# Performance work log

Measured on AMD Instinct MI355X. Metric: run time of the kernel, lower is better.

## Reference

```python
import jax, jax.numpy as jnp
import numpy as np

B, S, H, F, K = 32, 512, 256, 256, 3
NBINS, MAX_MEL = 256, 2048


def _conv1d(x, w, b):
    # x: [B,S,Cin], w: [K,Cin,Cout] -> [B,S,Cout], padding 1 (SAME, k=3)
    return jax.lax.conv_general_dilated(x, w, (1,), 'SAME',
        dimension_numbers=('NWC', 'WIO', 'NWC')) + b


def _ln(x, g, b):
    m = jnp.mean(x, -1, keepdims=True)
    v = jnp.var(x, -1, keepdims=True)
    return (x - m) * jax.lax.rsqrt(v + 1e-5) * g + b


def _predictor(x, mask, p):
    # FastSpeech2 VariancePredictor (eval mode, dropout off)
    w1, b1, g1, be1, w2, b2, g2, be2, wl, bl = p
    h = _ln(jax.nn.relu(_conv1d(x, w1, b1)), g1, be1)
    h = _ln(jax.nn.relu(_conv1d(h, w2, b2)), g2, be2)
    out = (h @ wl + bl)[..., 0]  # [B,S]
    return jnp.where(mask, 0.0, out)  # masked_fill(mask, 0.0)


def _make_predictor_params(key, out_bias):
    ks = jax.random.split(key, 3)
    w1 = jax.random.normal(ks[0], (K, H, F), jnp.float32) * 0.03
    w2 = jax.random.normal(ks[1], (K, F, F), jnp.float32) * 0.03
    wl = jax.random.normal(ks[2], (F, 1), jnp.float32) * 0.02
    return [w1, jnp.zeros((F,), jnp.float32), jnp.ones((F,), jnp.float32), jnp.zeros((F,), jnp.float32),
            w2, jnp.zeros((F,), jnp.float32), jnp.ones((F,), jnp.float32), jnp.zeros((F,), jnp.float32),
            wl, jnp.full((1,), out_bias, jnp.float32)]


PNAMES = ['w1', 'b1', 'g1', 'be1', 'w2', 'b2', 'g2', 'be2', 'wl', 'bl']


def setup_inputs() -> dict:
    key = jax.random.key(0)
    ks = jax.random.split(key, 8)
    inp = {
        'x': jax.random.normal(ks[0], (B, S, H), jnp.float32),
        'src_mask': jnp.zeros((B, S), jnp.bool_),  # True = padded position
        'pitch_control': jnp.float32(1.0),
        'energy_control': jnp.float32(1.0),
        'duration_control': jnp.float32(1.0),
        'pitch_bins': jnp.linspace(-4.0, 4.0, NBINS - 1, dtype=jnp.float32),
        'energy_bins': jnp.linspace(-4.0, 4.0, NBINS - 1, dtype=jnp.float32),
        'pitch_emb': jax.random.normal(ks[1], (NBINS, H), jnp.float32) * 0.02,
        'energy_emb': jax.random.normal(ks[2], (NBINS, H), jnp.float32) * 0.02,
    }
    # duration predictor output bias 1.6 ~ log(5) -> avg ~4 frames/phoneme
    for i, (pref, ob) in enumerate([('dur', 1.6), ('pit', 0.0), ('ene', 0.0)]):
        for n, v in zip(PNAMES, _make_predictor_params(ks[3 + i], ob)):
            inp[pref + '_' + n] = v
    return inp


def reference(x, src_mask, pitch_control, energy_control, duration_control,
              pitch_bins, energy_bins, pitch_emb, energy_emb,
              dur_w1, dur_b1, dur_g1, dur_be1, dur_w2, dur_b2, dur_g2, dur_be2, dur_wl, dur_bl,
              pit_w1, pit_b1, pit_g1, pit_be1, pit_w2, pit_b2, pit_g2, pit_be2, pit_wl, pit_bl,
              ene_w1, ene_b1, ene_g1, ene_be1, ene_w2, ene_b2, ene_g2, ene_be2, ene_wl, ene_bl):
    dur_p = [dur_w1, dur_b1, dur_g1, dur_be1, dur_w2, dur_b2, dur_g2, dur_be2, dur_wl, dur_bl]
    pit_p = [pit_w1, pit_b1, pit_g1, pit_be1, pit_w2, pit_b2, pit_g2, pit_be2, pit_wl, pit_bl]
    ene_p = [ene_w1, ene_b1, ene_g1, ene_be1, ene_w2, ene_b2, ene_g2, ene_be2, ene_wl, ene_bl]

    log_dur = _predictor(x, src_mask, dur_p)                      # [B,S]
    pitch_pred = _predictor(x, src_mask, pit_p) * pitch_control   # inference: scaled prediction
    # torch.bucketize(v, bins) (right=False) == searchsorted side='left'
    x = x + pitch_emb[jnp.searchsorted(pitch_bins, pitch_pred, side='left')]
    energy_pred = _predictor(x, src_mask, ene_p) * energy_control
    x = x + energy_emb[jnp.searchsorted(energy_bins, energy_pred, side='left')]

    dur = jnp.maximum(jnp.round(jnp.exp(log_dur) - 1.0) * duration_control, 0.0)  # [B,S]
    dur_i = dur.astype(jnp.int32)
    mel_len = jnp.minimum(jnp.sum(dur_i, -1), MAX_MEL)            # [B]
    # Length regulator: frame t maps to phoneme idx = #{cumdur <= t}
    cum = jnp.cumsum(dur_i, 1)                                    # [B,S]
    t = jnp.arange(MAX_MEL, dtype=jnp.int32)
    idx = jax.vmap(lambda c: jnp.searchsorted(c, t, side='right'))(cum)  # [B,MAX_MEL]
    idx = jnp.clip(idx, 0, S - 1)
    x_exp = jnp.take_along_axis(x, idx[:, :, None], axis=1)       # [B,MAX_MEL,H]
    mel_mask = t[None, :] >= mel_len[:, None]                     # True = padded frame
    x_exp = jnp.where(mel_mask[:, :, None], 0.0, x_exp)
    return (x_exp, pitch_pred, energy_pred, log_dur, dur, mel_len, mel_mask)
```

## Files before the change

### kernel.cpp

```cpp
#include <hip/hip_runtime.h>
#include <stdint.h>

#define BB 32
#define SS 512
#define HH 256
#define MM (BB*SS)
#define MAXMEL 2048

typedef _Float16 f16;
typedef _Float16 f16x4 __attribute__((ext_vector_type(4)));
typedef _Float16 f16x8 __attribute__((ext_vector_type(8)));
typedef float    f32x16 __attribute__((ext_vector_type(16)));

#define BAR()  asm volatile("s_barrier" ::: "memory")
#define VMW9() asm volatile("s_waitcnt vmcnt(9)" ::: "memory")
#define VMW0() asm volatile("s_waitcnt vmcnt(0)" ::: "memory")

__device__ __forceinline__ size_t xoff(int row, int chan) {
  int cb = chan >> 4, cc = (chan >> 3) & 1, e = chan & 7;
  return ((size_t)cb * MM + row) * 16 + (size_t)(((cc ^ (row & 1)) << 3) + e);
}

#define BBUF 24576
#define AOFF 49152
#define ABUF 12352
#define AZ   61440
#define LDSSZ 73856
#define WSZ  ((size_t)768*256)

template<int NS, int RAW>
__global__ __launch_bounds__(256) void conv16(
    const f16* __restrict__ X0h, const f16* __restrict__ X0l,
    const f16* __restrict__ X1h_, const f16* __restrict__ X1l_,
    const f16* __restrict__ W0h, const f16* __restrict__ W0l,
    const f16* __restrict__ W1h, const f16* __restrict__ W1l,
    const float* __restrict__ bias0, const float* __restrict__ bias1,
    f16* __restrict__ Y0h, f16* __restrict__ Y0l,
    f16* __restrict__ Y1h, f16* __restrict__ Y1l,
    float* __restrict__ Craw)
{
  __shared__ __align__(16) unsigned char smem[LDSSZ];
  const int tid = threadIdx.x;
  const int lane = tid & 63, wid = tid >> 6;
  const int bm = blockIdx.x, bn = blockIdx.y, bz = blockIdx.z;
  const int l31 = lane & 31, half = lane >> 5;
  const int hx4 = half << 4;
  const int wr = wid >> 1, wc = wid & 1;

  const int s0 = RAW ? bz * 8 : 0;
  const f16* Xh = (RAW || bz == 0) ? X0h : X1h_;
  const f16* Xl = (RAW || bz == 0) ? X0l : X1l_;
  const f16* Wh = (RAW || bz == 0) ? W0h : W1h;
  const f16* Wl = (RAW || bz == 0) ? W0l : W1l;

  const f16* sb[9]; int sdst[9]; int sstr[9]; int sdb[9];
  #pragma unroll
  for (int i = 0; i < 9; ++i) {
    int j = wid * 9 + i;
    if (j < 12) {
      int p = j / 6, seg = j % 6;
      int rowstart = bm * 128 - 32 + seg * 32;
      rowstart = rowstart < 0 ? 0 : (rowstart > MM - 32 ? MM - 32 : rowstart);
      sb[i]   = (p ? Xl : Xh) + (size_t)rowstart * 16 + lane * 8;
      sstr[i] = MM * 16;
      sdst[i] = AOFF + p * 6144 + seg * 1024 + lane * 16;
      sdb[i]  = ABUF;
    } else {
      int jj = j - 12;
      int p = jj / 12, tap = (jj % 12) / 4, q4 = jj & 3;
      sb[i]   = (p ? Wl : Wh) + ((size_t)(bn * 16) * 3 + tap) * 2048 + q4 * 512 + lane * 8;
      sstr[i] = 6144;
      sdst[i] = p * 12288 + tap * 4096 + q4 * 1024 + lane * 16;
      sdb[i]  = BBUF;
    }
  }

  int a_addr[3][2][2];
  #pragma unroll
  for (int tap = 0; tap < 3; ++tap)
    #pragma unroll
    for (int q = 0; q < 2; ++q) {
      int row_l = wr * 64 + q * 32 + l31;
      int s_t = (bm & 3) * 128 + row_l + tap - 1;
      bool valid = (unsigned)s_t < 512u;
      int lrow = row_l + tap + 31;
      int base = AOFF + lrow * 32 + ((lrow & 1) << 4);
      #pragma unroll
      for (int p = 0; p < 2; ++p)
        a_addr[tap][q][p] = valid ? (base + p * 6144) : AZ;
    }
  int b_base[2];
  #pragma unroll
  for (int n = 0; n < 2; ++n) {
    int col_l = wc * 64 + n * 32 + l31;
    b_base[n] = col_l * 32 + ((col_l & 1) << 4);
  }

  f32x16 acc[2][2];
  #pragma unroll
  for (int mi = 0; mi < 2; ++mi)
    #pragma unroll
    for (int ni = 0; ni < 2; ++ni) acc[mi][ni] = (f32x16)0.f;

  auto STAGE = [&](int buf, int step) {
    #pragma unroll
    for (int i = 0; i < 9; ++i)
      __builtin_amdgcn_global_load_lds(
        (const __attribute__((address_space(1))) void*)(sb[i] + (size_t)step * sstr[i]),
        (__attribute__((address_space(3))) void*)(smem + sdst[i] + buf * sdb[i]),
        16, 0, 0);
  };

  auto COMP = [&](int buf) {
    #pragma unroll
    for (int tap = 0; tap < 3; ++tap) {
      f16x8 av[2][2], bv[2][2];
      #pragma unroll
      for (int p = 0; p < 2; ++p)
        #pragma unroll
        for (int q = 0; q < 2; ++q) {
          av[p][q] = *(const f16x8*)(smem + ((a_addr[tap][q][p] ^ hx4) + buf * ABUF));
          bv[p][q] = *(const f16x8*)(smem + (buf * BBUF + p * 12288 + tap * 4096 + (b_base[q] ^ hx4)));
        }
      #pragma unroll
      for (int mi = 0; mi < 2; ++mi)
        #pragma unroll
        for (int ni = 0; ni < 2; ++ni) {
          acc[mi][ni] = __builtin_amdgcn_mfma_f32_32x32x16_f16(av[0][mi], bv[0][ni], acc[mi][ni], 0, 0, 0);
          acc[mi][ni] = __builtin_amdgcn_mfma_f32_32x32x16_f16(av[0][mi], bv[1][ni], acc[mi][ni], 0, 0, 0);
          acc[mi][ni] = __builtin_amdgcn_mfma_f32_32x32x16_f16(av[1][mi], bv[0][ni], acc[mi][ni], 0, 0, 0);
        }
    }
  };

  if (tid < 4) {
    *(float4*)(smem + AZ + tid * 16) = make_float4(0.f, 0.f, 0.f, 0.f);
    *(float4*)(smem + AZ + ABUF + tid * 16) = make_float4(0.f, 0.f, 0.f, 0.f);
  }
  STAGE(0, s0); STAGE(1, s0 + 1);
  __syncthreads();

  #pragma unroll
  for (int i = 0; i < NS; ++i) {
    COMP(i & 1);
    BAR();
    if (i < NS - 2)       { STAGE(i & 1, s0 + i + 2); VMW9(); }
    else if (i == NS - 2) { VMW0(); }
    BAR();
  }

  if constexpr (RAW) {
    float* C = Craw + (size_t)bz * MM * 256;
    #pragma unroll
    for (int mi = 0; mi < 2; ++mi)
      #pragma unroll
      for (int ni = 0; ni < 2; ++ni) {
        int colg = bn * 128 + wc * 64 + ni * 32 + l31;
        #pragma unroll
        for (int r = 0; r < 16; ++r) {
          int rowl = (r & 3) + 8 * (r >> 2) + 4 * half;
          size_t rowg = (size_t)bm * 128 + wr * 64 + mi * 32 + rowl;
          C[rowg * 256 + colg] = acc[mi][ni][r];
        }
      }
  } else {
    const float* bias = bz ? bias1 : bias0;
    f16* Yh = bz ? Y1h : Y0h;
    f16* Yl = bz ? Y1l : Y0l;
    #pragma unroll
    for (int mi = 0; mi < 2; ++mi)
      #pragma unroll
      for (int ni = 0; ni < 2; ++ni) {
        int colg = bn * 128 + wc * 64 + ni * 32 + l31;
        float bvs = bias[colg];
        int cb = colg >> 4, cc = (colg >> 3) & 1, e = colg & 7;
        #pragma unroll
        for (int r = 0; r < 16; ++r) {
          int rowl = (r & 3) + 8 * (r >> 2) + 4 * half;
          int rowg = bm * 128 + wr * 64 + mi * 32 + rowl;
          float v = fmaxf(acc[mi][ni][r] + bvs, 0.f);
          f16 h = (f16)v;
          f16 l = (f16)(v - (float)h);
          size_t o = ((size_t)cb * MM + rowg) * 16 + ((cc ^ (rowg & 1)) << 3) + e;
          Yh[o] = h;
          Yl[o] = l;
        }
      }
  }
}

__global__ __launch_bounds__(256) void wsplit6(
    const float* __restrict__ W0, const float* __restrict__ W1,
    const float* __restrict__ W2, const float* __restrict__ W3,
    const float* __restrict__ W4, const float* __restrict__ W5,
    f16* __restrict__ Wt)
{
  int z = blockIdx.y;
  const float* W = z==0?W0 : z==1?W1 : z==2?W2 : z==3?W3 : z==4?W4 : W5;
  f16* Thi = Wt + (size_t)z * 2 * WSZ;
  f16* Tlo = Thi + WSZ;
  int id = blockIdx.x * 256 + threadIdx.x;
  int slot = id & 1, col = (id >> 1) & 127;
  int t3 = id >> 8;
  int tap = t3 % 3, bs = t3 / 3;
  int step = bs & 15, bnn = bs >> 4;
  int gg = slot ^ (col & 1);
  int chan = step * 16 + gg * 8;
  int colg = bnn * 128 + col;
  f16x8 hi, lo;
  #pragma unroll
  for (int e = 0; e < 8; ++e) {
    float w = W[(size_t)(tap * 256 + chan + e) * 256 + colg];
    f16 h = (f16)w;
    hi[e] = h;
    lo[e] = (f16)(w - (float)h);
  }
  *(f16x8*)(Thi + (size_t)id * 8) = hi;
  *(f16x8*)(Tlo + (size_t)id * 8) = lo;
}

__global__ __launch_bounds__(256) void split2(
    const float* __restrict__ X, f16* __restrict__ Hi, f16* __restrict__ Lo)
{
  int id = blockIdx.x * 256 + threadIdx.x;
  int row = id >> 5, chan = (id & 31) * 8;
  const float* src = X + (size_t)row * 256 + chan;
  float4 v0 = *(const float4*)src;
  float4 v1 = *(const float4*)(src + 4);
  float vv[8] = {v0.x, v0.y, v0.z, v0.w, v1.x, v1.y, v1.z, v1.w};
  f16x8 h, l;
  #pragma unroll
  for (int j = 0; j < 8; ++j) {
    f16 hh = (f16)vv[j];
    h[j] = hh;
    l[j] = (f16)(vv[j] - (float)hh);
  }
  size_t o = xoff(row, chan);
  *(f16x8*)(Hi + o) = h;
  *(f16x8*)(Lo + o) = l;
}

__global__ __launch_bounds__(256) void lnF(
    f16* __restrict__ P0h, f16* __restrict__ P0l,
    f16* __restrict__ P1h, f16* __restrict__ P1l,
    const float* __restrict__ g0, const float* __restrict__ be0,
    const float* __restrict__ g1, const float* __restrict__ be1)
{
  int z = blockIdx.y;
  f16* Ph = z ? P1h : P0h;
  f16* Pl = z ? P1l : P0l;
  const float* g  = z ? g1 : g0;
  const float* be = z ? be1 : be0;
  int row  = blockIdx.x * 4 + (threadIdx.x >> 6);
  int lane = threadIdx.x & 63;
  size_t o = xoff(row, lane * 4);
  f16x4 h = *(const f16x4*)(Ph + o);
  f16x4 l = *(const f16x4*)(Pl + o);
  float v[4];
  #pragma unroll
  for (int j = 0; j < 4; ++j) v[j] = (float)h[j] + (float)l[j];
  float s = v[0] + v[1] + v[2] + v[3];
  float q = v[0]*v[0] + v[1]*v[1] + v[2]*v[2] + v[3]*v[3];
  #pragma unroll
  for (int d = 32; d > 0; d >>= 1) { s += __shfl_xor(s, d); q += __shfl_xor(q, d); }
  float mean = s * (1.f / 256.f);
  float var  = q * (1.f / 256.f) - mean * mean;
  float inv  = 1.0f / sqrtf(var + 1e-5f);
  float4 gg = *(const float4*)(g + lane * 4);
  float4 bb = *(const float4*)(be + lane * 4);
  float gv[4] = {gg.x, gg.y, gg.z, gg.w};
  float bv[4] = {bb.x, bb.y, bb.z, bb.w};
  #pragma unroll
  for (int j = 0; j < 4; ++j) {
    float oo = (v[j] - mean) * inv * gv[j] + bv[j];
    f16 hh = (f16)oo;
    h[j] = hh;
    l[j] = (f16)(oo - (float)hh);
  }
  *(f16x4*)(Ph + o) = h;
  *(f16x4*)(Pl + o) = l;
}

__global__ __launch_bounds__(256) void lnheadD(
    const f16* __restrict__ U0h, const f16* __restrict__ U0l,
    const f16* __restrict__ U1h, const f16* __restrict__ U1l,
    const float* __restrict__ g0, const float* __restrict__ be0,
    const float* __restrict__ wl0, const float* __restrict__ bl0,
    const float* __restrict__ g1, const float* __restrict__ be1,
    const float* __restrict__ wl1, const float* __restrict__ bl1,
    const unsigned char* __restrict__ mask, const float* __restrict__ pc,
    float* __restrict__ o_ldur, float* __restrict__ pred_d,
    float* __restrict__ o_pit,
    const float* __restrict__ pbins, const float* __restrict__ pemb,
    const f16* __restrict__ XPh, const f16* __restrict__ XPl,
    f16* __restrict__ X1h, f16* __restrict__ X1l)
{
  int z = blockIdx.y;
  int row  = blockIdx.x * 4 + (threadIdx.x >> 6);
  int lane = threadIdx.x & 63;
  size_t o = xoff(row, lane * 4);
  const f16* Uh = z ? U1h : U0h;
  const f16* Ul = z ? U1l : U0l;
  f16x4 h = *(const f16x4*)(Uh + o);
  f16x4 l = *(const f16x4*)(Ul + o);
  float v[4];
  #pragma unroll
  for (int j = 0; j < 4; ++j) v[j] = (float)h[j] + (float)l[j];
  float s = v[0] + v[1] + v[2] + v[3];
  float q = v[0]*v[0] + v[1]*v[1] + v[2]*v[2] + v[3]*v[3];
  #pragma unroll
  for (int d = 32; d > 0; d >>= 1) { s += __shfl_xor(s, d); q += __shfl_xor(q, d); }
  float mean = s * (1.f / 256.f);
  float var  = q * (1.f / 256.f) - mean * mean;
  float inv  = 1.0f / sqrtf(var + 1e-5f);
  const float* g  = z ? g1  : g0;
  const float* be = z ? be1 : be0;
  const float* wl = z ? wl1 : wl0;
  float4 gg = *(const float4*)(g + lane * 4);
  float4 bb = *(const float4*)(be + lane * 4);
  float4 ww = *(const float4*)(wl + lane * 4);
  float gv[4] = {gg.x, gg.y, gg.z, gg.w};
  float bv[4] = {bb.x, bb.y, bb.z, bb.w};
  float wv[4] = {ww.x, ww.y, ww.z, ww.w};
  float acc = 0.f;
  #pragma unroll
  for (int j = 0; j < 4; ++j)
    acc += ((v[j] - mean) * inv * gv[j] + bv[j]) * wv[j];
  #pragma unroll
  for (int d = 32; d > 0; d >>= 1) acc += __shfl_xor(acc, d);
  float r = acc + (z ? bl1 : bl0)[0];
  if (mask[row]) r = 0.f;
  if (z == 0) {
    if (lane == 0) { o_ldur[row] = r; pred_d[row] = r; }
  } else {
    r *= pc[0];
    if (lane == 0) o_pit[row] = r;
    int lo = 0, hi = 255;
    while (lo < hi) { int mid = (lo + hi) >> 1; if (pbins[mid] < r) lo = mid + 1; else hi = mid; }
    f16x4 xh = *(const f16x4*)(XPh + o);
    f16x4 xl = *(const f16x4*)(XPl + o);
    float4 e = *(const float4*)(pemb + (size_t)lo * HH + lane * 4);
    float ev[4] = {e.x, e.y, e.z, e.w};
    #pragma unroll
    for (int j = 0; j < 4; ++j) {
      float oo = (float)xh[j] + (float)xl[j] + ev[j];
      f16 hh = (f16)oo;
      xh[j] = hh;
      xl[j] = (f16)(oo - (float)hh);
    }
    *(f16x4*)(X1h + o) = xh;
    *(f16x4*)(X1l + o) = xl;
  }
}

__global__ __launch_bounds__(256) void lnS(
    const float* __restrict__ C0, const float* __restrict__ C1,
    const float* __restrict__ bias,
    const float* __restrict__ g, const float* __restrict__ be,
    f16* __restrict__ Yh, f16* __restrict__ Yl)
{
  int row  = blockIdx.x * 4 + (threadIdx.x >> 6);
  int lane = threadIdx.x & 63;
  size_t ci = (size_t)row * 256 + lane * 4;
  float4 a = *(const float4*)(C0 + ci);
  float4 b = *(const float4*)(C1 + ci);
  float4 bs = *(const float4*)(bias + lane * 4);
  float v[4] = {fmaxf(a.x + b.x + bs.x, 0.f), fmaxf(a.y + b.y + bs.y, 0.f),
                fmaxf(a.z + b.z + bs.z, 0.f), fmaxf(a.w + b.w + bs.w, 0.f)};
  float s = v[0] + v[1] + v[2] + v[3];
  float q = v[0]*v[0] + v[1]*v[1] + v[2]*v[2] + v[3]*v[3];
  #pragma unroll
  for (int d = 32; d > 0; d >>= 1) { s += __shfl_xor(s, d); q += __shfl_xor(q, d); }
  float mean = s * (1.f / 256.f);
  float var  = q * (1.f / 256.f) - mean * mean;
  float inv  = 1.0f / sqrtf(var + 1e-5f);
  float4 gg = *(const float4*)(g + lane * 4);
  float4 bb = *(const float4*)(be + lane * 4);
  float gv[4] = {gg.x, gg.y, gg.z, gg.w};
  float bv[4] = {bb.x, bb.y, bb.z, bb.w};
  f16x4 h, l;
  #pragma unroll
  for (int j = 0; j < 4; ++j) {
    float oo = (v[j] - mean) * inv * gv[j] + bv[j];
    f16 hh = (f16)oo;
    h[j] = hh;
    l[j] = (f16)(oo - (float)hh);
  }
  size_t o = xoff(row, lane * 4);
  *(f16x4*)(Yh + o) = h;
  *(f16x4*)(Yl + o) = l;
}

__global__ __launch_bounds__(256) void lnheadS(
    const float* __restrict__ C0, const float* __restrict__ C1,
    const float* __restrict__ bias,
    const float* __restrict__ g, const float* __restrict__ be,
    const float* __restrict__ wl, const float* __restrict__ bl,
    const unsigned char* __restrict__ mask, const float* __restrict__ ec,
    float* __restrict__ o_ene,
    const float* __restrict__ ebins, const float* __restrict__ eemb,
    const f16* __restrict__ X1h, const f16* __restrict__ X1l,
    f16* __restrict__ X2h, f16* __restrict__ X2l)
{
  int row  = blockIdx.x * 4 + (threadIdx.x >> 6);
  int lane = threadIdx.x & 63;
  size_t ci = (size_t)row * 256 + lane * 4;
  float4 a = *(const float4*)(C0 + ci);
  float4 b = *(const float4*)(C1 + ci);
  float4 bs = *(const float4*)(bias + lane * 4);
  float v[4] = {fmaxf(a.x + b.x + bs.x, 0.f), fmaxf(a.y + b.y + bs.y, 0.f),
                fmaxf(a.z + b.z + bs.z, 0.f), fmaxf(a.w + b.w + bs.w, 0.f)};
  float s = v[0] + v[1] + v[2] + v[3];
  float q = v[0]*v[0] + v[1]*v[1] + v[2]*v[2] + v[3]*v[3];
  #pragma unroll
  for (int d = 32; d > 0; d >>= 1) { s += __shfl_xor(s, d); q += __shfl_xor(q, d); }
  float mean = s * (1.f / 256.f);
  float var  = q * (1.f / 256.f) - mean * mean;
  float inv  = 1.0f / sqrtf(var + 1e-5f);
  float4 gg = *(const float4*)(g + lane * 4);
  float4 bb = *(const float4*)(be + lane * 4);
  float4 ww = *(const float4*)(wl + lane * 4);
  float gv[4] = {gg.x, gg.y, gg.z, gg.w};
  float bv[4] = {bb.x, bb.y, bb.z, bb.w};
  float wv[4] = {ww.x, ww.y, ww.z, ww.w};
  float acc = 0.f;
  #pragma unroll
  for (int j = 0; j < 4; ++j)
    acc += ((v[j] - mean) * inv * gv[j] + bv[j]) * wv[j];
  #pragma unroll
  for (int d = 32; d > 0; d >>= 1) acc += __shfl_xor(acc, d);
  float r = acc + bl[0];
  if (mask[row]) r = 0.f;
  r *= ec[0];
  if (lane == 0) o_ene[row] = r;
  int lo = 0, hi = 255;
  while (lo < hi) { int mid = (lo + hi) >> 1; if (ebins[mid] < r) lo = mid + 1; else hi = mid; }
  size_t o = xoff(row, lane * 4);
  f16x4 xh = *(const f16x4*)(X1h + o);
  f16x4 xl = *(const f16x4*)(X1l + o);
  float4 e = *(const float4*)(eemb + (size_t)lo * HH + lane * 4);
  float ev[4] = {e.x, e.y, e.z, e.w};
  #pragma unroll
  for (int j = 0; j < 4; ++j) {
    float oo = (float)xh[j] + (float)xl[j] + ev[j];
    f16 hh = (f16)oo;
    xh[j] = hh;
    xl[j] = (f16)(oo - (float)hh);
  }
  *(f16x4*)(X2h + o) = xh;
  *(f16x4*)(X2l + o) = xl;
}

__global__ __launch_bounds__(512) void dur_post(
    const float* __restrict__ logdur, const float* __restrict__ dc,
    float* __restrict__ out_dur, float* __restrict__ out_mel_len,
    int* __restrict__ cum_ws, int* __restrict__ mel_len_ws)
{
  __shared__ int wsum[8];
  int b = blockIdx.x, t = threadIdx.x;
  float ld = logdur[b * SS + t];
  float d  = fmaxf(rintf(expf(ld) - 1.f) * dc[0], 0.f);
  out_dur[b * SS + t] = d;
  int di = (int)d;
  int lane = t & 63, w = t >> 6;
  int x = di;
  #pragma unroll
  for (int dd = 1; dd < 64; dd <<= 1) {
    int n = __shfl_up(x, dd);
    if (lane >= dd) x += n;
  }
  if (lane == 63) wsum[w] = x;
  __syncthreads();
  int off = 0;
  for (int i = 0; i < w; ++i) off += wsum[i];
  x += off;
  cum_ws[b * SS + t] = x;
  if (t == SS - 1) {
    int ml = min(x, MAXMEL);
    mel_len_ws[b] = ml;
    out_mel_len[b] = (float)ml;
  }
}

__global__ __launch_bounds__(256) void gather_planes(
    const f16* __restrict__ Xhi, const f16* __restrict__ Xlo,
    const int* __restrict__ cum, const int* __restrict__ mel_len_ws,
    float* __restrict__ out_x, float* __restrict__ out_mask)
{
  __shared__ int c[SS];
  int b   = blockIdx.y;
  int tid = threadIdx.x;
  c[tid]       = cum[b * SS + tid];
  c[tid + 256] = cum[b * SS + tid + 256];
  __syncthreads();
  int w = tid >> 6, lane = tid & 63;
  int t = blockIdx.x * 4 + w;
  int lo = 0, hi = SS;
  while (lo < hi) { int mid = (lo + hi) >> 1; if (c[mid] <= t) lo = mid + 1; else hi = mid; }
  int idx = min(lo, SS - 1);
  int ml  = mel_len_ws[b];
  bool m  = (t >= ml);
  float4 v = make_float4(0.f, 0.f, 0.f, 0.f);
  if (!m) {
    size_t o = xoff(b * SS + idx, lane * 4);
    f16x4 xh = *(const f16x4*)(Xhi + o);
    f16x4 xl = *(const f16x4*)(Xlo + o);
    v.x = (float)xh[0] + (float)xl[0];
    v.y = (float)xh[1] + (float)xl[1];
    v.z = (float)xh[2] + (float)xl[2];
    v.w = (float)xh[3] + (float)xl[3];
  }
  *(float4*)(out_x + ((size_t)b * MAXMEL + t) * HH + lane * 4) = v;
  if (lane == 0) out_mask[b * MAXMEL + t] = m ? 1.f : 0.f;
}

extern "C" void kernel_launch(void* const* d_in, const int* in_sizes, int n_in,
                              void* d_out, int out_size, void* d_ws, size_t ws_size,
                              hipStream_t stream) {
  const float* x     = (const float*)d_in[0];
  const unsigned char* smask = (const unsigned char*)d_in[1];
  const float* pc    = (const float*)d_in[2];
  const float* ec    = (const float*)d_in[3];
  const float* dc    = (const float*)d_in[4];
  const float* pbins = (const float*)d_in[5];
  const float* ebins = (const float*)d_in[6];
  const float* pemb  = (const float*)d_in[7];
  const float* eemb  = (const float*)d_in[8];

  float* out = (float*)d_out;
  float* o_xexp  = out;
  float* o_pit   = out + (size_t)16777216;
  float* o_ene   = o_pit + 16384;
  float* o_ldur  = o_ene + 16384;
  float* o_dur   = o_ldur + 16384;
  float* o_mlen  = o_dur + 16384;
  float* o_mmask = o_mlen + 32;

  const size_t PL = (size_t)MM * HH;
  f16* p = (f16*)d_ws;
  f16 *XPh = p, *XPl = p + PL;
  f16 *Tdh = p + 2*PL, *Tdl = p + 3*PL;
  f16 *Tph = p + 4*PL, *Tpl = p + 5*PL;
  f16 *Udh = p + 6*PL, *Udl = p + 7*PL;
  f16 *Uph = p + 8*PL, *Upl = p + 9*PL;
  f16 *X1h = p + 10*PL, *X1l = p + 11*PL;
  f16 *Teh = p + 12*PL, *Tel = p + 13*PL;
  f16 *X2h = p + 14*PL, *X2l = p + 15*PL;
  f16* Wt  = p + 16*PL;
  float* C0 = (float*)(Wt + 12 * WSZ);
  float* C1 = C0 + (size_t)MM * 256;
  float* pred_d = C1 + (size_t)MM * 256;
  int*   cum = (int*)(pred_d + MM);
  int*   mlw = cum + MM;

  #define WPH(i) (Wt + (size_t)(i) * 2 * WSZ)
  #define WPL(i) (Wt + (size_t)(i) * 2 * WSZ + WSZ)

  wsplit6<<<dim3(96, 6), 256, 0, stream>>>(
      (const float*)d_in[9], (const float*)d_in[13], (const float*)d_in[19],
      (const float*)d_in[23], (const float*)d_in[29], (const float*)d_in[33], Wt);

  split2<<<2048, 256, 0, stream>>>(x, XPh, XPl);

  dim3 cgrid(128, 2, 2);
  dim3 rgrid(MM / 4);
  dim3 rgrid2(MM / 4, 2);

  conv16<16, 0><<<cgrid, 256, 0, stream>>>(
      XPh, XPl, XPh, XPl,
      WPH(0), WPL(0), WPH(2), WPL(2),
      (const float*)d_in[10], (const float*)d_in[20],
      Tdh, Tdl, Tph, Tpl, nullptr);
  lnF<<<rgrid2, 256, 0, stream>>>(Tdh, Tdl, Tph, Tpl,
      (const float*)d_in[11], (const float*)d_in[12],
      (const float*)d_in[21], (const float*)d_in[22]);
  conv16<16, 0><<<cgrid, 256, 0, stream>>>(
      Tdh, Tdl, Tph, Tpl,
      WPH(1), WPL(1), WPH(3), WPL(3),
      (const float*)d_in[14], (const float*)d_in[24],
      Udh, Udl, Uph, Upl, nullptr);
  lnheadD<<<rgrid2, 256, 0, stream>>>(
      Udh, Udl, Uph, Upl,
      (const float*)d_in[15], (const float*)d_in[16],
      (const float*)d_in[17], (const float*)d_in[18],
      (const float*)d_in[25], (const float*)d_in[26],
      (const float*)d_in[27], (const float*)d_in[28],
      smask, pc, o_ldur, pred_d, o_pit, pbins, pemb,
      XPh, XPl, X1h, X1l);
  dur_post<<<BB, 512, 0, stream>>>(pred_d, dc, o_dur, o_mlen, cum, mlw);

  conv16<8, 1><<<cgrid, 256, 0, stream>>>(
      X1h, X1l, X1h, X1l,
      WPH(4), WPL(4), WPH(4), WPL(4),
      nullptr, nullptr, nullptr, nullptr, nullptr, nullptr, C0);
  lnS<<<rgrid, 256, 0, stream>>>(C0, C1, (const float*)d_in[30],
      (const float*)d_in[31], (const float*)d_in[32], Teh, Tel);
  conv16<8, 1><<<cgrid, 256, 0, stream>>>(
      Teh, Tel, Teh, Tel,
      WPH(5), WPL(5), WPH(5), WPL(5),
      nullptr, nullptr, nullptr, nullptr, nullptr, nullptr, C0);
  lnheadS<<<rgrid, 256, 0, stream>>>(C0, C1, (const float*)d_in[34],
      (const float*)d_in[35], (const float*)d_in[36],
      (const float*)d_in[37], (const float*)d_in[38],
      smask, ec, o_ene, ebins, eemb, X1h, X1l, X2h, X2l);

  dim3 ggrid(MAXMEL / 4, BB);
  gather_planes<<<ggrid, 256, 0, stream>>>(X2h, X2l, cum, mlw, o_xexp, o_mmask);

  #undef WPH
  #undef WPL
}
```

Before: 231.3 us.

## Shrink conv tiles to 64 rows, single-buffer LDS, drop split-K energy path

The conv kernel moves from 128x128 tiles with double-buffered LDS to 64x128 tiles with a single buffer. LDS use drops to about 32KB, and launch bounds request 4 blocks per CU, so occupancy rather than software pipelining hides load latency. The activation layout becomes a row-pair swizzle, and the weight-split kernel is updated to match. The energy predictor no longer uses a split-K fp32 partial-sum path followed by a reduction LN kernel; it runs the same fused bias+ReLU conv as the other predictors. This trades load/compute overlap inside a block for more resident blocks and less fp32 intermediate traffic.

```diff
diff --git a/kernel.cpp b/kernel.cpp
--- a/kernel.cpp
+++ b/kernel.cpp
@@ -13,31 +13,29 @@
 typedef float    f32x16 __attribute__((ext_vector_type(16)));
 
 #define BAR()  asm volatile("s_barrier" ::: "memory")
-#define VMW9() asm volatile("s_waitcnt vmcnt(9)" ::: "memory")
 #define VMW0() asm volatile("s_waitcnt vmcnt(0)" ::: "memory")
 
 __device__ __forceinline__ size_t xoff(int row, int chan) {
-  int cb = chan >> 4, cc = (chan >> 3) & 1, e = chan & 7;
-  return ((size_t)cb * MM + row) * 16 + (size_t)(((cc ^ (row & 1)) << 3) + e);
-}
-
-#define BBUF 24576
-#define AOFF 49152
-#define ABUF 12352
-#define AZ   61440
-#define LDSSZ 73856
-#define WSZ  ((size_t)768*256)
-
-template<int NS, int RAW>
-__global__ __launch_bounds__(256) void conv16(
+  int cb = chan >> 4, g = (chan >> 3) & 1, e = chan & 7;
+  int rp = row >> 1, par = row & 1;
+  int slot = (2 * par + g) ^ ((rp >> 1) & 3);
+  return (((size_t)cb * (MM / 2) + rp) * 4 + slot) * 8 + e;
+}
+
+#define BOFF  0
+#define AOFF  24576
+#define AZ    32768
+#define LDSSZ 32832
+#define WSZ   ((size_t)768 * 256)
+
+__global__ __launch_bounds__(256, 4) void conv64(
     const f16* __restrict__ X0h, const f16* __restrict__ X0l,
     const f16* __restrict__ X1h_, const f16* __restrict__ X1l_,
     const f16* __restrict__ W0h, const f16* __restrict__ W0l,
     const f16* __restrict__ W1h, const f16* __restrict__ W1l,
     const float* __restrict__ bias0, const float* __restrict__ bias1,
     f16* __restrict__ Y0h, f16* __restrict__ Y0l,
-    f16* __restrict__ Y1h, f16* __restrict__ Y1l,
-    float* __restrict__ Craw)
+    f16* __restrict__ Y1h, f16* __restrict__ Y1l)
 {
   __shared__ __align__(16) unsigned char smem[LDSSZ];
   const int tid = threadIdx.x;
@@ -47,145 +45,122 @@
   const int hx4 = half << 4;
   const int wr = wid >> 1, wc = wid & 1;
 
-  const int s0 = RAW ? bz * 8 : 0;
-  const f16* Xh = (RAW || bz == 0) ? X0h : X1h_;
-  const f16* Xl = (RAW || bz == 0) ? X0l : X1l_;
-  const f16* Wh = (RAW || bz == 0) ? W0h : W1h;
-  const f16* Wl = (RAW || bz == 0) ? W0l : W1l;
-
-  const f16* sb[9]; int sdst[9]; int sstr[9]; int sdb[9];
-  #pragma unroll
-  for (int i = 0; i < 9; ++i) {
-    int j = wid * 9 + i;
-    if (j < 12) {
-      int p = j / 6, seg = j % 6;
-      int rowstart = bm * 128 - 32 + seg * 32;
+  const f16* Xh = bz ? X1h_ : X0h;
+  const f16* Xl = bz ? X1l_ : X0l;
+  const f16* Wh = bz ? W1h : W0h;
+  const f16* Wl = bz ? W1l : W0l;
+
+  const f16* sb[8]; int sdst[8];
+  size_t sstr;
+  #pragma unroll
+  for (int i = 0; i < 8; ++i) {
+    int j = wid * 8 + i;
+    if (j < 8) {
+      int p = j >> 2, seg = j & 3;
+      int rowstart = bm * 64 - 32 + seg * 32;
       rowstart = rowstart < 0 ? 0 : (rowstart > MM - 32 ? MM - 32 : rowstart);
-      sb[i]   = (p ? Xl : Xh) + (size_t)rowstart * 16 + lane * 8;
-      sstr[i] = MM * 16;
-      sdst[i] = AOFF + p * 6144 + seg * 1024 + lane * 16;
-      sdb[i]  = ABUF;
+      sb[i]   = (p ? Xl : Xh) + (size_t)(rowstart >> 1) * 32 + lane * 8;
+      sdst[i] = AOFF + p * 4096 + seg * 1024 + lane * 16;
     } else {
-      int jj = j - 12;
-      int p = jj / 12, tap = (jj % 12) / 4, q4 = jj & 3;
-      sb[i]   = (p ? Wl : Wh) + ((size_t)(bn * 16) * 3 + tap) * 2048 + q4 * 512 + lane * 8;
-      sstr[i] = 6144;
-      sdst[i] = p * 12288 + tap * 4096 + q4 * 1024 + lane * 16;
-      sdb[i]  = BBUF;
+      int jj = j - 8;
+      int tap = jj >> 3, rem = jj & 7;
+      int p = rem >> 2, q4 = rem & 3;
+      sb[i]   = (p ? Wl : Wh) + ((size_t)((bn * 16) * 3 + tap) * 256 + q4 * 64 + lane) * 8;
+      sdst[i] = tap * 8192 + p * 4096 + q4 * 1024 + lane * 16;
     }
   }
-
-  int a_addr[3][2][2];
-  #pragma unroll
-  for (int tap = 0; tap < 3; ++tap)
+  sstr = (wid == 0) ? (size_t)(MM / 2) * 32 : (size_t)3 * 256 * 8;
+
+  int a_addr[3][2];
+  #pragma unroll
+  for (int tap = 0; tap < 3; ++tap) {
+    int row_l = wr * 32 + l31;
+    int sseq = (bm & 7) * 64 + row_l + tap - 1;
+    bool valid = (unsigned)sseq < 512u;
+    int lrow = row_l + tap + 31;
+    int rp = lrow >> 1, par = lrow & 1;
+    int slot0 = (2 * par) ^ ((rp >> 1) & 3);
+    int base = AOFF + rp * 64 + slot0 * 16;
+    a_addr[tap][0] = valid ? base : AZ;
+    a_addr[tap][1] = valid ? (base + 4096) : AZ;
+  }
+  int b_base[2];
+  #pragma unroll
+  for (int n = 0; n < 2; ++n) {
+    int col = wc * 64 + n * 32 + l31;
+    int cp = col >> 1, cpar = col & 1;
+    int slot0 = (2 * cpar) ^ ((cp >> 1) & 3);
+    b_base[n] = cp * 64 + slot0 * 16;
+  }
+
+  f32x16 acc[2];
+  acc[0] = (f32x16)0.f;
+  acc[1] = (f32x16)0.f;
+
+  auto STAGE = [&](int step) {
     #pragma unroll
-    for (int q = 0; q < 2; ++q) {
-      int row_l = wr * 64 + q * 32 + l31;
-      int s_t = (bm & 3) * 128 + row_l + tap - 1;
-      bool valid = (unsigned)s_t < 512u;
-      int lrow = row_l + tap + 31;
-      int base = AOFF + lrow * 32 + ((lrow & 1) << 4);
-      #pragma unroll
-      for (int p = 0; p < 2; ++p)
-        a_addr[tap][q][p] = valid ? (base + p * 6144) : AZ;
-    }
-  int b_base[2];
-  #pragma unroll
-  for (int n = 0; n < 2; ++n) {
-    int col_l = wc * 64 + n * 32 + l31;
-    b_base[n] = col_l * 32 + ((col_l & 1) << 4);
-  }
-
-  f32x16 acc[2][2];
-  #pragma unroll
-  for (int mi = 0; mi < 2; ++mi)
-    #pragma unroll
-    for (int ni = 0; ni < 2; ++ni) acc[mi][ni] = (f32x16)0.f;
-
-  auto STAGE = [&](int buf, int step) {
-    #pragma unroll
-    for (int i = 0; i < 9; ++i)
+    for (int i = 0; i < 8; ++i)
       __builtin_amdgcn_global_load_lds(
-        (const __attribute__((address_space(1))) void*)(sb[i] + (size_t)step * sstr[i]),
-        (__attribute__((address_space(3))) void*)(smem + sdst[i] + buf * sdb[i]),
-        16, 0, 0);
+        (const __attribute__((address_space(1))) void*)(sb[i] + (size_t)step * sstr),
+        (__attribute__((address_space(3))) void*)(smem + sdst[i]), 16, 0, 0);
   };
 
-  auto COMP = [&](int buf) {
+  auto COMP = [&]() {
     #pragma unroll
     for (int tap = 0; tap < 3; ++tap) {
-      f16x8 av[2][2], bv[2][2];
+      f16x8 av[2], bv[2][2];
       #pragma unroll
-      for (int p = 0; p < 2; ++p)
+      for (int p = 0; p < 2; ++p) {
+        av[p] = *(const f16x8*)(smem + (a_addr[tap][p] ^ hx4));
         #pragma unroll
-        for (int q = 0; q < 2; ++q) {
-          av[p][q] = *(const f16x8*)(smem + ((a_addr[tap][q][p] ^ hx4) + buf * ABUF));
-          bv[p][q] = *(const f16x8*)(smem + (buf * BBUF + p * 12288 + tap * 4096 + (b_base[q] ^ hx4)));
-        }
+        for (int n = 0; n < 2; ++n)
+          bv[p][n] = *(const f16x8*)(smem + (tap * 8192 + p * 4096 + (b_base[n] ^ hx4)));
+      }
       #pragma unroll
-      for (int mi = 0; mi < 2; ++mi)
-        #pragma unroll
-        for (int ni = 0; ni < 2; ++ni) {
-          acc[mi][ni] = __builtin_amdgcn_mfma_f32_32x32x16_f16(av[0][mi], bv[0][ni], acc[mi][ni], 0, 0, 0);
-          acc[mi][ni] = __builtin_amdgcn_mfma_f32_32x32x16_f16(av[0][mi], bv[1][ni], acc[mi][ni], 0, 0, 0);
-          acc[mi][ni] = __builtin_amdgcn_mfma_f32_32x32x16_f16(av[1][mi], bv[0][ni], acc[mi][ni], 0, 0, 0);
-        }
+      for (int n = 0; n < 2; ++n) {
+        acc[n] = __builtin_amdgcn_mfma_f32_32x32x16_f16(av[0], bv[0][n], acc[n], 0, 0, 0);
+        acc[n] = __builtin_amdgcn_mfma_f32_32x32x16_f16(av[0], bv[1][n], acc[n], 0, 0, 0);
+        acc[n] = __builtin_amdgcn_mfma_f32_32x32x16_f16(av[1], bv[0][n], acc[n], 0, 0, 0);
+      }
     }
   };
 
-  if (tid < 4) {
+  if (tid < 4)
     *(float4*)(smem + AZ + tid * 16) = make_float4(0.f, 0.f, 0.f, 0.f);
-    *(float4*)(smem + AZ + ABUF + tid * 16) = make_float4(0.f, 0.f, 0.f, 0.f);
-  }
-  STAGE(0, s0); STAGE(1, s0 + 1);
+  STAGE(0);
   __syncthreads();
 
-  #pragma unroll
-  for (int i = 0; i < NS; ++i) {
-    COMP(i & 1);
-    BAR();
-    if (i < NS - 2)       { STAGE(i & 1, s0 + i + 2); VMW9(); }
-    else if (i == NS - 2) { VMW0(); }
-    BAR();
-  }
-
-  if constexpr (RAW) {
-    float* C = Craw + (size_t)bz * MM * 256;
+  for (int i = 0; i < 16; ++i) {
+    COMP();
+    if (i < 15) {
+      BAR();
+      STAGE(i + 1);
+      VMW0();
+      BAR();
+    }
+  }
+
+  const float* bias = bz ? bias1 : bias0;
+  f16* Yh = bz ? Y1h : Y0h;
+  f16* Yl = bz ? Y1l : Y0l;
+  #pragma unroll
+  for (int n = 0; n < 2; ++n) {
+    int colg = bn * 128 + wc * 64 + n * 32 + l31;
+    float bvs = bias[colg];
+    int cb = colg >> 4, g = (colg >> 3) & 1, e = colg & 7;
     #pragma unroll
-    for (int mi = 0; mi < 2; ++mi)
-      #pragma unroll
-      for (int ni = 0; ni < 2; ++ni) {
-        int colg = bn * 128 + wc * 64 + ni * 32 + l31;
-        #pragma unroll
-        for (int r = 0; r < 16; ++r) {
-          int rowl = (r & 3) + 8 * (r >> 2) + 4 * half;
-          size_t rowg = (size_t)bm * 128 + wr * 64 + mi * 32 + rowl;
-          C[rowg * 256 + colg] = acc[mi][ni][r];
-        }
-      }
-  } else {
-    const float* bias = bz ? bias1 : bias0;
-    f16* Yh = bz ? Y1h : Y0h;
-    f16* Yl = bz ? Y1l : Y0l;
-    #pragma unroll
-    for (int mi = 0; mi < 2; ++mi)
-      #pragma unroll
-      for (int ni = 0; ni < 2; ++ni) {
-        int colg = bn * 128 + wc * 64 + ni * 32 + l31;
-        float bvs = bias[colg];
-        int cb = colg >> 4, cc = (colg >> 3) & 1, e = colg & 7;
-        #pragma unroll
-        for (int r = 0; r < 16; ++r) {
-          int rowl = (r & 3) + 8 * (r >> 2) + 4 * half;
-          int rowg = bm * 128 + wr * 64 + mi * 32 + rowl;
-          float v = fmaxf(acc[mi][ni][r] + bvs, 0.f);
-          f16 h = (f16)v;
-          f16 l = (f16)(v - (float)h);
-          size_t o = ((size_t)cb * MM + rowg) * 16 + ((cc ^ (rowg & 1)) << 3) + e;
-          Yh[o] = h;
-          Yl[o] = l;
-        }
-      }
+    for (int r = 0; r < 16; ++r) {
+      int rowl = (r & 3) + 8 * (r >> 2) + 4 * half;
+      int rowg = bm * 64 + wr * 32 + rowl;
+      float v = fmaxf(acc[n][r] + bvs, 0.f);
+      f16 h = (f16)v;
+      f16 l = (f16)(v - (float)h);
+      int rp = rowg >> 1, par = rowg & 1;
+      int slot = (2 * par + g) ^ ((rp >> 1) & 3);
+      size_t o = (((size_t)cb * (MM / 2) + rp) * 4 + slot) * 8 + e;
+      Yh[o] = h;
+      Yl[o] = l;
+    }
   }
 }
 
@@ -200,12 +175,14 @@
   f16* Thi = Wt + (size_t)z * 2 * WSZ;
   f16* Tlo = Thi + WSZ;
   int id = blockIdx.x * 256 + threadIdx.x;
-  int slot = id & 1, col = (id >> 1) & 127;
+  int slot = id & 3, cp = (id >> 2) & 63;
   int t3 = id >> 8;
   int tap = t3 % 3, bs = t3 / 3;
   int step = bs & 15, bnn = bs >> 4;
-  int gg = slot ^ (col & 1);
-  int chan = step * 16 + gg * 8;
+  int s2 = slot ^ ((cp >> 1) & 3);
+  int cpar = s2 >> 1, g = s2 & 1;
+  int col = cp * 2 + cpar;
+  int chan = step * 16 + g * 8;
   int colg = bnn * 128 + col;
   f16x8 hi, lo;
   #pragma unroll
@@ -353,47 +330,8 @@
   }
 }
 
-__global__ __launch_bounds__(256) void lnS(
-    const float* __restrict__ C0, const float* __restrict__ C1,
-    const float* __restrict__ bias,
-    const float* __restrict__ g, const float* __restrict__ be,
-    f16* __restrict__ Yh, f16* __restrict__ Yl)
-{
-  int row  = blockIdx.x * 4 + (threadIdx.x >> 6);
-  int lane = threadIdx.x & 63;
-  size_t ci = (size_t)row * 256 + lane * 4;
-  float4 a = *(const float4*)(C0 + ci);
-  float4 b = *(const float4*)(C1 + ci);
-  float4 bs = *(const float4*)(bias + lane * 4);
-  float v[4] = {fmaxf(a.x + b.x + bs.x, 0.f), fmaxf(a.y + b.y + bs.y, 0.f),
-                fmaxf(a.z + b.z + bs.z, 0.f), fmaxf(a.w + b.w + bs.w, 0.f)};
-  float s = v[0] + v[1] + v[2] + v[3];
-  float q = v[0]*v[0] + v[1]*v[1] + v[2]*v[2] + v[3]*v[3];
-  #pragma unroll
-  for (int d = 32; d > 0; d >>= 1) { s += __shfl_xor(s, d); q += __shfl_xor(q, d); }
-  float mean = s * (1.f / 256.f);
-  float var  = q * (1.f / 256.f) - mean * mean;
-  float inv  = 1.0f / sqrtf(var + 1e-5f);
-  float4 gg = *(const float4*)(g + lane * 4);
-  float4 bb = *(const float4*)(be + lane * 4);
-  float gv[4] = {gg.x, gg.y, gg.z, gg.w};
-  float bv[4] = {bb.x, bb.y, bb.z, bb.w};
-  f16x4 h, l;
-  #pragma unroll
-  for (int j = 0; j < 4; ++j) {
-    float oo = (v[j] - mean) * inv * gv[j] + bv[j];
-    f16 hh = (f16)oo;
-    h[j] = hh;
-    l[j] = (f16)(oo - (float)hh);
-  }
-  size_t o = xoff(row, lane * 4);
-  *(f16x4*)(Yh + o) = h;
-  *(f16x4*)(Yl + o) = l;
-}
-
-__global__ __launch_bounds__(256) void lnheadS(
-    const float* __restrict__ C0, const float* __restrict__ C1,
-    const float* __restrict__ bias,
+__global__ __launch_bounds__(256) void lnheadE(
+    const f16* __restrict__ Uh, const f16* __restrict__ Ul,
     const float* __restrict__ g, const float* __restrict__ be,
     const float* __restrict__ wl, const float* __restrict__ bl,
     const unsigned char* __restrict__ mask, const float* __restrict__ ec,
@@ -404,12 +342,12 @@
 {
   int row  = blockIdx.x * 4 + (threadIdx.x >> 6);
   int lane = threadIdx.x & 63;
-  size_t ci = (size_t)row * 256 + lane * 4;
-  float4 a = *(const float4*)(C0 + ci);
-  float4 b = *(const float4*)(C1 + ci);
-  float4 bs = *(const float4*)(bias + lane * 4);
-  float v[4] = {fmaxf(a.x + b.x + bs.x, 0.f), fmaxf(a.y + b.y + bs.y, 0.f),
-                fmaxf(a.z + b.z + bs.z, 0.f), fmaxf(a.w + b.w + bs.w, 0.f)};
+  size_t o = xoff(row, lane * 4);
+  f16x4 h = *(const f16x4*)(Uh + o);
+  f16x4 l = *(const f16x4*)(Ul + o);
+  float v[4];
+  #pragma unroll
+  for (int j = 0; j < 4; ++j) v[j] = (float)h[j] + (float)l[j];
   float s = v[0] + v[1] + v[2] + v[3];
   float q = v[0]*v[0] + v[1]*v[1] + v[2]*v[2] + v[3]*v[3];
   #pragma unroll
@@ -435,7 +373,6 @@
   if (lane == 0) o_ene[row] = r;
   int lo = 0, hi = 255;
   while (lo < hi) { int mid = (lo + hi) >> 1; if (ebins[mid] < r) lo = mid + 1; else hi = mid; }
-  size_t o = xoff(row, lane * 4);
   f16x4 xh = *(const f16x4*)(X1h + o);
   f16x4 xl = *(const f16x4*)(X1l + o);
   float4 e = *(const float4*)(eemb + (size_t)lo * HH + lane * 4);
@@ -538,18 +475,17 @@
 
   const size_t PL = (size_t)MM * HH;
   f16* p = (f16*)d_ws;
-  f16 *XPh = p, *XPl = p + PL;
+  f16 *XPh = p,        *XPl = p + PL;
   f16 *Tdh = p + 2*PL, *Tdl = p + 3*PL;
   f16 *Tph = p + 4*PL, *Tpl = p + 5*PL;
   f16 *Udh = p + 6*PL, *Udl = p + 7*PL;
   f16 *Uph = p + 8*PL, *Upl = p + 9*PL;
   f16 *X1h = p + 10*PL, *X1l = p + 11*PL;
   f16 *Teh = p + 12*PL, *Tel = p + 13*PL;
-  f16 *X2h = p + 14*PL, *X2l = p + 15*PL;
-  f16* Wt  = p + 16*PL;
-  float* C0 = (float*)(Wt + 12 * WSZ);
-  float* C1 = C0 + (size_t)MM * 256;
-  float* pred_d = C1 + (size_t)MM * 256;
+  f16 *Ueh = p + 14*PL, *Uel = p + 15*PL;
+  f16 *X2h = p + 16*PL, *X2l = p + 17*PL;
+  f16* Wt  = p + 18*PL;
+  float* pred_d = (float*)(Wt + 12 * WSZ);
   int*   cum = (int*)(pred_d + MM);
   int*   mlw = cum + MM;
 
@@ -562,23 +498,24 @@
 
   split2<<<2048, 256, 0, stream>>>(x, XPh, XPl);
 
-  dim3 cgrid(128, 2, 2);
+  dim3 cgrid2(256, 2, 2);
+  dim3 cgrid1(256, 2, 1);
   dim3 rgrid(MM / 4);
   dim3 rgrid2(MM / 4, 2);
 
-  conv16<16, 0><<<cgrid, 256, 0, stream>>>(
+  conv64<<<cgrid2, 256, 0, stream>>>(
       XPh, XPl, XPh, XPl,
       WPH(0), WPL(0), WPH(2), WPL(2),
       (const float*)d_in[10], (const float*)d_in[20],
-      Tdh, Tdl, Tph, Tpl, nullptr);
+      Tdh, Tdl, Tph, Tpl);
   lnF<<<rgrid2, 256, 0, stream>>>(Tdh, Tdl, Tph, Tpl,
       (const float*)d_in[11], (const float*)d_in[12],
       (const float*)d_in[21], (const float*)d_in[22]);
-  conv16<16, 0><<<cgrid, 256, 0, stream>>>(
+  conv64<<<cgrid2, 256, 0, stream>>>(
       Tdh, Tdl, Tph, Tpl,
       WPH(1), WPL(1), WPH(3), WPL(3),
       (const float*)d_in[14], (const float*)d_in[24],
-      Udh, Udl, Uph, Upl, nullptr);
+      Udh, Udl, Uph, Upl);
   lnheadD<<<rgrid2, 256, 0, stream>>>(
       Udh, Udl, Uph, Upl,
       (const float*)d_in[15], (const float*)d_in[16],
@@ -589,17 +526,20 @@
       XPh, XPl, X1h, X1l);
   dur_post<<<BB, 512, 0, stream>>>(pred_d, dc, o_dur, o_mlen, cum, mlw);
 
-  conv16<8, 1><<<cgrid, 256, 0, stream>>>(
+  conv64<<<cgrid1, 256, 0, stream>>>(
       X1h, X1l, X1h, X1l,
       WPH(4), WPL(4), WPH(4), WPL(4),
-      nullptr, nullptr, nullptr, nullptr, nullptr, nullptr, C0);
-  lnS<<<rgrid, 256, 0, stream>>>(C0, C1, (const float*)d_in[30],
-      (const float*)d_in[31], (const float*)d_in[32], Teh, Tel);
-  conv16<8, 1><<<cgrid, 256, 0, stream>>>(
+      (const float*)d_in[30], (const float*)d_in[30],
+      Teh, Tel, Teh, Tel);
+  lnF<<<dim3(MM / 4, 1), 256, 0, stream>>>(Teh, Tel, Teh, Tel,
+      (const float*)d_in[31], (const float*)d_in[32],
+      (const float*)d_in[31], (const float*)d_in[32]);
+  conv64<<<cgrid1, 256, 0, stream>>>(
       Teh, Tel, Teh, Tel,
       WPH(5), WPL(5), WPH(5), WPL(5),
-      nullptr, nullptr, nullptr, nullptr, nullptr, nullptr, C0);
-  lnheadS<<<rgrid, 256, 0, stream>>>(C0, C1, (const float*)d_in[34],
+      (const float*)d_in[34], (const float*)d_in[34],
+      Ueh, Uel, Ueh, Uel);
+  lnheadE<<<rgrid, 256, 0, stream>>>(Ueh, Uel,
       (const float*)d_in[35], (const float*)d_in[36],
       (const float*)d_in[37], (const float*)d_in[38],
       smask, ec, o_ene, ebins, eemb, X1h, X1l, X2h, X2l);
```

Result: slower. 248.1 us (+7.2%).
